# Optimization experiments

Hardware: AMD Instinct MI355X
Metric: run time of the kernel (lower is better)

Reference implementation:

```python
import jax, jax.numpy as jnp
import numpy as np

V, E, HD, H, T = 50000, 256, 512, 256, 50  # vocab, embed, hidden_dim, per-direction hidden, tagset
B, S = 128, 512


def setup_inputs() -> dict:
    key = jax.random.key(0)
    ks = jax.random.split(key, 16)
    def n(k, shape, s=0.05):
        return jax.random.normal(k, shape, dtype=jnp.float32) * s
    return {
        "sentences": jax.random.randint(ks[0], (B, S), 0, V),
        "tags": jax.random.randint(ks[1], (B, S), 0, T),
        "mask": jnp.ones((B, S), dtype=bool),
        "embedding": n(ks[2], (V, E), 0.1),
        "w_ih_f": n(ks[3], (4 * H, E)), "w_hh_f": n(ks[4], (4 * H, H)),
        "b_ih_f": n(ks[5], (4 * H,)), "b_hh_f": n(ks[6], (4 * H,)),
        "w_ih_b": n(ks[7], (4 * H, E)), "w_hh_b": n(ks[8], (4 * H, H)),
        "b_ih_b": n(ks[9], (4 * H,)), "b_hh_b": n(ks[10], (4 * H,)),
        "W_out": n(ks[11], (T, HD)), "b_out": n(ks[12], (T,)),
        "start_trans": n(ks[13], (T,), 0.1),
        "end_trans": n(ks[14], (T,), 0.1),
        "trans": n(ks[15], (T, T), 0.1),
    }


def _lstm(xs, w_ih, w_hh, b, reverse):
    # xs: [S, B, E]; PyTorch gate order i, f, g, o
    Hn = w_hh.shape[1]
    def cell(carry, xt):
        h, c = carry
        g = xt @ w_ih.T + h @ w_hh.T + b
        i, f, gg, o = jnp.split(g, 4, axis=-1)
        c = jax.nn.sigmoid(f) * c + jax.nn.sigmoid(i) * jnp.tanh(gg)
        h = jax.nn.sigmoid(o) * jnp.tanh(c)
        return (h, c), h
    z = jnp.zeros((xs.shape[1], Hn), xs.dtype)
    _, hs = jax.lax.scan(cell, (z, z), xs, reverse=reverse)
    return hs  # [S, B, Hn], time-aligned with xs


def reference(sentences, tags, mask, embedding, w_ih_f, w_hh_f, b_ih_f, b_hh_f,
              w_ih_b, w_hh_b, b_ih_b, b_hh_b, W_out, b_out,
              start_trans, end_trans, trans):
    xs = jnp.swapaxes(embedding[sentences], 0, 1)           # [S, B, E]
    hf = _lstm(xs, w_ih_f, w_hh_f, b_ih_f + b_hh_f, False)
    hb = _lstm(xs, w_ih_b, w_hh_b, b_ih_b + b_hh_b, True)
    emis = jnp.concatenate([hf, hb], -1) @ W_out.T + b_out  # [S, B, T]

    tagsT = jnp.swapaxes(tags, 0, 1)                        # [S, B]
    maskT = jnp.swapaxes(mask, 0, 1)                        # [S, B] bool
    mT = maskT.astype(emis.dtype)

    # --- numerator: score of the gold path (first timestep always on, per torchcrf) ---
    emit = jnp.take_along_axis(emis, tagsT[..., None], axis=-1)[..., 0]   # [S, B]
    num = start_trans[tagsT[0]] + emit[0]
    num = num + jnp.sum((trans[tagsT[:-1], tagsT[1:]] + emit[1:]) * mT[1:], axis=0)
    last = jnp.sum(maskT.astype(jnp.int32), axis=0) - 1                    # [B]
    num = num + end_trans[tags[jnp.arange(tags.shape[0]), last]]

    # --- denominator: log-partition via forward algorithm (logsumexp scan) ---
    alpha0 = start_trans[None, :] + emis[0]                 # [B, T]
    def step(alpha, inp):
        e_t, m_t = inp
        nxt = jax.nn.logsumexp(alpha[:, :, None] + trans[None] + e_t[:, None, :], axis=1)
        return jnp.where(m_t[:, None], nxt, alpha), None
    alpha, _ = jax.lax.scan(step, alpha0, (emis[1:], maskT[1:]))
    logZ = jax.nn.logsumexp(alpha + end_trans[None, :], axis=1)

    # model returns -crf(...) with reduction='mean'
    return -jnp.mean(num - logZ)
```

## Files before the change

kernel.cpp:

```cpp
#include <hip/hip_runtime.h>

typedef __bf16 bf16x8 __attribute__((ext_vector_type(8)));
typedef float f32x4 __attribute__((ext_vector_type(4)));
typedef float f32x2 __attribute__((ext_vector_type(2)));
typedef int i32x8 __attribute__((ext_vector_type(8)));
typedef unsigned short ushort_t;
typedef unsigned int u32x4 __attribute__((ext_vector_type(4)));
typedef long i64_t;

constexpr int Ee = 256;
constexpr int HDd = 512;
constexpr int Hh = 256;
constexpr int Tt = 50;
constexpr int Bb = 128;
constexpr int Ss = 512;
constexpr int G4 = 1024;
constexpr int SB = Ss * Bb;
constexpr int Tc = 64;
constexpr int NP = Ss / Tc;
constexpr int HSTR = 272;
constexpr int NSLOT = 16;

constexpr float LOG2E = 1.4426950408889634f;
constexpr float K2f = 2.8853900817779268f;

#define DI __device__ __forceinline__

DI float bf2f(ushort_t u) {
    unsigned int x = ((unsigned int)u) << 16;
    return __builtin_bit_cast(float, x);
}
DI ushort_t f2bf(float f) {
    unsigned int x = __builtin_bit_cast(unsigned int, f);
    x += 0x7fffu + ((x >> 16) & 1u);
    return (ushort_t)(x >> 16);
}
DI bf16x8 cvt8(const float* p) {
    bf16x8 r;
#pragma unroll
    for (int i = 0; i < 8; ++i) r[i] = (__bf16)p[i];
    return r;
}
DI unsigned int pk4_fp8(float a, float b, float c, float d) {
    int v = __builtin_amdgcn_cvt_pk_fp8_f32(a, b, 0, false);
    v = __builtin_amdgcn_cvt_pk_fp8_f32(c, d, v, true);
    return (unsigned int)v;
}
DI unsigned char fp8_1(float a) {
    return (unsigned char)(__builtin_amdgcn_cvt_pk_fp8_f32(a, 0.f, 0, false) & 0xff);
}
DI float rcpf(float x) { return __builtin_amdgcn_rcpf(x); }

#if __has_builtin(__builtin_amdgcn_exp2f)
DI float ex2(float x) { return __builtin_amdgcn_exp2f(x); }
DI float ex2n(float x) { return __builtin_amdgcn_exp2f(-x); }
#else
DI float ex2(float x) {
    float r;
    asm("v_exp_f32 %0, %1\n\ts_nop 0" : "=v"(r) : "v"(x));
    return r;
}
DI float ex2n(float x) {
    float r;
    asm("v_exp_f32 %0, -%1\n\ts_nop 0" : "=v"(r) : "v"(x));
    return r;
}
#endif

DI void lds_barrier() {
    asm volatile("" ::: "memory");
    __builtin_amdgcn_s_waitcnt(0xC07F);
    __builtin_amdgcn_s_barrier();
    asm volatile("" ::: "memory");
}

__global__ void k_prep(const float* __restrict__ wihf, const float* __restrict__ whhf,
                       const float* __restrict__ wihb, const float* __restrict__ whhb,
                       const float* __restrict__ wout,
                       const float* __restrict__ bihf, const float* __restrict__ bhhf,
                       const float* __restrict__ bihb, const float* __restrict__ bhhb,
                       ushort_t* __restrict__ Wihf, ushort_t* __restrict__ Wihb,
                       unsigned char* __restrict__ Whhf8, unsigned char* __restrict__ Whhb8,
                       unsigned char* __restrict__ Wout8,
                       float* __restrict__ biasf, float* __restrict__ biasb,
                       unsigned int* __restrict__ flags) {
    int i = blockIdx.x * 256 + threadIdx.x;
    if (i < G4 * Ee) {
        float s = (((i >> 16) & 3) == 2) ? K2f : LOG2E;
        Wihf[i] = f2bf(wihf[i] * s);
        Wihb[i] = f2bf(wihb[i] * s);
    }
    if (i < G4 * Hh / 4) {
        int base = i * 4;
        float s = (((i >> 14) & 3) == 2) ? K2f : LOG2E;
        ((unsigned int*)Whhf8)[i] = pk4_fp8(whhf[base] * s, whhf[base + 1] * s,
                                            whhf[base + 2] * s, whhf[base + 3] * s);
        ((unsigned int*)Whhb8)[i] = pk4_fp8(whhb[base] * s, whhb[base + 1] * s,
                                            whhb[base + 2] * s, whhb[base + 3] * s);
    }
    if (i < 64 * HDd) Wout8[i] = 0;
    if (i < Tt * HDd) Wout8[i] = fp8_1(wout[i]);
    if (i < G4) {
        float s = (((i >> 8) & 3) == 2) ? K2f : LOG2E;
        biasf[i] = (bihf[i] + bhhf[i]) * s;
        biasb[i] = (bihb[i] + bhhb[i]) * s;
    }
    if (i < 32) flags[i] = 0;
}

struct PhaseArgs {
    const int* sentences;
    const int* tags;
    const float* emb;
    const ushort_t* Wihf;
    const ushort_t* Wihb;
    const float* biasf;
    const float* biasb;
    const unsigned char* Whhf8;
    const unsigned char* Whhb8;
    const unsigned char* Wout8;
    const float* bout;
    const float* start_trans;
    const float* end_trans;
    const float* trans;
    unsigned char* Gbuf;
    unsigned char* Hcat8;
    float* emis;
    float* logZ;
    float* num;
    float* out;
    unsigned int* flags;
};

__global__ __launch_bounds__(512, 2) void k_phase(PhaseArgs a) {
    __shared__ unsigned char hring[NSLOT][16][HSTR];
    const size_t CH = (size_t)Tc * Bb * G4;
    int blk = blockIdx.x;
    int tid = threadIdx.x;

    if (blk < 16) {
        int ln = tid & 15, qd = (tid >> 4) & 3, w = tid >> 6;
        int dir = blk >> 3;
        int b0 = (blk & 7) * 16;
        const unsigned char* Whh8 = dir ? a.Whhb8 : a.Whhf8;
        int jc0 = w * 32 + ln;

        i32x8 wreg[2][4][2];
#pragma unroll
        for (int ct = 0; ct < 2; ++ct)
#pragma unroll
            for (int g = 0; g < 4; ++g) {
                const unsigned char* wb = Whh8 + (size_t)(g * Hh + jc0 + ct * 16) * Hh;
#pragma unroll
                for (int ks = 0; ks < 2; ++ks)
                    wreg[ct][g][ks] = *(const i32x8*)(wb + ks * 128 + qd * 32);
            }
        for (int i = tid; i < NSLOT * 16 * HSTR; i += 512) ((unsigned char*)hring)[i] = 0;
        __syncthreads();
        float creg[2][4] = {};
        int sctr = 0;

        for (int p = 0; p < NP; ++p) {
            if (tid == 0) {
                while (__hip_atomic_load(&a.flags[p], __ATOMIC_RELAXED,
                                         __HIP_MEMORY_SCOPE_AGENT) < 240u)
                    __builtin_amdgcn_s_sleep(1);
                __threadfence();
            }
            __syncthreads();

            const unsigned char* G = a.Gbuf + ((size_t)(dir * 2 + (p & 1))) * CH;
            int goff = ((dir ? (Tc - 1) : 0) * 32 + (b0 >> 2) + qd) * 4096 + jc0 * 16;
            const int gstep = dir ? -(32 * 4096) : (32 * 4096);

            u32x4 guA[2], guB[2];
#pragma unroll
            for (int ct = 0; ct < 2; ++ct)
                guA[ct] = *(const u32x4*)(G + goff + ct * 256);

            auto lstm_step = [&](u32x4(&gcur)[2], u32x4(&gnxt)[2], int step) {
                int rslot = (sctr + NSLOT - 1) & (NSLOT - 1), wslot = sctr & (NSLOT - 1);
                int goff2 = goff + gstep;
                if (step + 1 < Tc) {
#pragma unroll
                    for (int ct = 0; ct < 2; ++ct)
                        gnxt[ct] = *(const u32x4*)(G + goff2 + ct * 256);
                }
                i32x8 av2[2];
#pragma unroll
                for (int ks = 0; ks < 2; ++ks)
                    av2[ks] = *(const i32x8*)&hring[rslot][ln][ks * 128 + qd * 32];
                f32x4 acc[2][4];
#pragma unroll
                for (int ct = 0; ct < 2; ++ct)
#pragma unroll
                    for (int g = 0; g < 4; ++g) {
                        f32x2 lo = __builtin_amdgcn_cvt_pk_f32_fp8((int)gcur[ct][g], false);
                        f32x2 hi = __builtin_amdgcn_cvt_pk_f32_fp8((int)gcur[ct][g], true);
                        acc[ct][g][0] = lo[0];
                        acc[ct][g][1] = lo[1];
                        acc[ct][g][2] = hi[0];
                        acc[ct][g][3] = hi[1];
                    }
#pragma unroll
                for (int ks = 0; ks < 2; ++ks)
#pragma unroll
                    for (int ct = 0; ct < 2; ++ct)
#pragma unroll
                        for (int g = 0; g < 4; ++g)
                            acc[ct][g] = __builtin_amdgcn_mfma_scale_f32_16x16x128_f8f6f4(
                                av2[ks], wreg[ct][g][ks], acc[ct][g],
                                0, 0,
                                0, 127,
                                0, 127);
#pragma unroll
                for (int ct = 0; ct < 2; ++ct)
#pragma unroll
                    for (int reg = 0; reg < 4; ++reg) {
                        float ei = ex2n(acc[ct][0][reg]);
                        float ef = ex2n(acc[ct][1][reg]);
                        float eg = ex2(acc[ct][2][reg]);
                        float eo = ex2n(acc[ct][3][reg]);
                        float pf = 1.f + ef;
                        float pig = (1.f + ei) * (eg + 1.f);
                        float t2 = fmaf(eg, K2f, -K2f);
                        float cn = fmaf(creg[ct][reg], pig, t2 * pf) * rcpf(pf * pig);
                        creg[ct][reg] = cn;
                        float ec = ex2(cn);
                        float h = (ec - 1.f) * rcpf((1.f + eo) * (ec + 1.f));
                        hring[wslot][qd * 4 + reg][jc0 + ct * 16] = fp8_1(h);
                    }
                goff = goff2;
                lds_barrier();

                if ((sctr & 7) == 7) {
                    int tbase = sctr - 7;
                    int rid = tid >> 2;
                    int slotidx = rid >> 4, m = rid & 15;
                    int slot = (tbase + slotidx) & (NSLOT - 1);
                    int qp = tid & 3;
                    int t = dir ? (511 - (tbase + slotidx)) : (tbase + slotidx);
                    const unsigned char* src = &hring[slot][m][qp * 64];
                    unsigned char* dst = a.Hcat8 + ((size_t)(t * Bb + b0 + m)) * HDd + dir * Hh + qp * 64;
#pragma unroll
                    for (int i2 = 0; i2 < 4; ++i2) {
                        u32x4 v;
#pragma unroll
                        for (int k = 0; k < 4; ++k)
                            v[k] = *(const unsigned int*)(src + i2 * 16 + k * 4);
                        *(u32x4*)(dst + i2 * 16) = v;
                    }
                }
                ++sctr;
            };

            for (int step = 0; step < Tc; step += 2) {
                lstm_step(guA, guB, step);
                lstm_step(guB, guA, step + 1);
            }

            __syncthreads();
            if (tid == 0) {
                if (p == NP - 1) __threadfence();
                atomicAdd(&a.flags[8 + p], 1u);
            }
        }
    } else {
        int team = tid >> 8;
        int stid = tid & 255;
        int slot = (blk - 16) * 2 + team;
        int ln = stid & 15, qd = (stid >> 4) & 3, wv = stid >> 6;
        for (int q = 0; q < NP; ++q) {
            if (q >= 2) {
                if (tid == 0)
                    while (__hip_atomic_load(&a.flags[8 + q - 2], __ATOMIC_RELAXED,
                                             __HIP_MEMORY_SCOPE_AGENT) < 16u)
                        __builtin_amdgcn_s_sleep(64);
                __syncthreads();
            }
            for (int tile = slot; tile < 1024; tile += 480) {
                int dir = tile >> 9;
                int rem = tile & 511;
                int rt0 = rem >> 3, ct0 = rem & 7;
                const ushort_t* W = dir ? a.Wihb : a.Wihf;
                const float* bias = dir ? a.biasb : a.biasf;
                unsigned char* Gout = a.Gbuf + ((size_t)(dir * 2 + (q & 1))) * CH;
                int t0 = dir ? (NP - 1 - q) * Tc : q * Tc;
                int r0 = rt0 * 128 + (wv & 1) * 64;
                int n0 = ct0 * 128 + (wv >> 1) * 64;
                const float* aptr[4];
#pragma unroll
                for (int rt = 0; rt < 4; ++rt) {
                    int r = r0 + rt * 16 + ln;
                    int t = t0 + (r >> 7), b = r & 127;
                    aptr[rt] = a.emb + (size_t)a.sentences[b * Ss + t] * Ee;
                }
                int wrow[4];
#pragma unroll
                for (int ct = 0; ct < 4; ++ct) {
                    int c = n0 + ct * 16 + ln;
                    wrow[ct] = (c & 3) * 256 + (c >> 2);
                }
                f32x4 acc[4][4] = {};
                for (int ks = 0; ks < 8; ++ks) {
                    int k0 = ks * 32 + qd * 8;
                    bf16x8 av[4], bfr[4];
#pragma unroll
                    for (int rt = 0; rt < 4; ++rt) av[rt] = cvt8(aptr[rt] + k0);
#pragma unroll
                    for (int ct = 0; ct < 4; ++ct)
                        bfr[ct] = *(const bf16x8*)(W + (size_t)wrow[ct] * Ee + k0);
#pragma unroll
                    for (int rt = 0; rt < 4; ++rt)
#pragma unroll
                        for (int ct = 0; ct < 4; ++ct)
                            acc[rt][ct] = __builtin_amdgcn_mfma_f32_16x16x32_bf16(av[rt], bfr[ct], acc[rt][ct], 0, 0, 0);
                }
#pragma unroll
                for (int rt = 0; rt < 4; ++rt)
#pragma unroll
                    for (int ct = 0; ct < 4; ++ct) {
                        int c = n0 + ct * 16 + ln;
                        float bv = bias[wrow[ct]];
                        unsigned int pk = pk4_fp8(acc[rt][ct][0] + bv, acc[rt][ct][1] + bv,
                                                  acc[rt][ct][2] + bv, acc[rt][ct][3] + bv);
                        int rowq = ((r0 + rt * 16) >> 2) + qd;
                        *(unsigned int*)(Gout + (size_t)rowq * 4096 + (size_t)c * 4) = pk;
                    }
            }
            __syncthreads();
            if (tid == 0) {
                __threadfence();
                atomicAdd(&a.flags[q], 1u);
            }
        }
    }

    if (tid == 0) {
        while (__hip_atomic_load(&a.flags[15], __ATOMIC_RELAXED,
                                 __HIP_MEMORY_SCOPE_AGENT) < 16u)
            __builtin_amdgcn_s_sleep(16);
        __threadfence();
    }
    __syncthreads();
    {
        int ln = tid & 15, qd = (tid >> 4) & 3, w = tid >> 6;
        int r0 = blk * 256 + w * 32;
        f32x4 acc[2][4] = {};
        for (int ks = 0; ks < 16; ++ks) {
            int k0 = ks * 32 + qd * 8;
            i64_t av[2], bfr[4];
#pragma unroll
            for (int rt = 0; rt < 2; ++rt)
                av[rt] = *(const i64_t*)(a.Hcat8 + (size_t)(r0 + rt * 16 + ln) * HDd + k0);
#pragma unroll
            for (int ct = 0; ct < 4; ++ct)
                bfr[ct] = *(const i64_t*)(a.Wout8 + (size_t)(ct * 16 + ln) * HDd + k0);
#pragma unroll
            for (int rt = 0; rt < 2; ++rt)
#pragma unroll
                for (int ct = 0; ct < 4; ++ct)
                    acc[rt][ct] = __builtin_amdgcn_mfma_f32_16x16x32_fp8_fp8(av[rt], bfr[ct], acc[rt][ct], 0, 0, 0);
        }
#pragma unroll
        for (int rt = 0; rt < 2; ++rt)
#pragma unroll
            for (int ct = 0; ct < 4; ++ct) {
                int j = ct * 16 + ln;
                if (j < Tt) {
                    float bv = a.bout[j];
#pragma unroll
                    for (int reg = 0; reg < 4; ++reg) {
                        int row = r0 + rt * 16 + qd * 4 + reg;
                        int t = row >> 7, b = row & 127;
                        a.emis[((size_t)b * Ss + t) * Tt + j] = acc[rt][ct][reg] + bv;
                    }
                }
            }
    }
    __syncthreads();
    if (tid == 0) {
        __threadfence();
        atomicAdd(&a.flags[16], 1u);
        while (__hip_atomic_load(&a.flags[16], __ATOMIC_RELAXED,
                                 __HIP_MEMORY_SCOPE_AGENT) < 256u)
            __builtin_amdgcn_s_sleep(16);
        __threadfence();
    }
    __syncthreads();

    if (blk < 128) {
        if (tid < 64) {
            float* E_s = (float*)&hring[0][0][0];
            int j = tid;
            int b = blk;
            const float* eb = a.emis + (size_t)b * Ss * Tt;

            float preg[52];
            preg[50] = 0.f;
            preg[51] = 0.f;
#pragma unroll
            for (int i = 0; i < Tt; ++i)
                preg[i] = (j < Tt) ? __expf(a.trans[i * Tt + j]) : 0.f;

            float astart = (j < Tt) ? (a.start_trans[j] + eb[j]) : 0.f;
            float a0 = __builtin_amdgcn_readfirstlane(astart);
            float vcur = (j < Tt) ? __expf(astart - a0) : 0.f;
            float logacc = a0;
            E_s[j] = vcur;

            float ecur[8], enxt[8];
#pragma unroll
            for (int i = 0; i < 8; ++i)
                ecur[i] = (j < Tt && 1 + i < Ss) ? eb[(1 + i) * Tt + j] : 0.f;

            for (int tb = 1; tb < Ss; tb += 8) {
#pragma unroll
                for (int i = 0; i < 8; ++i) {
                    int tn = tb + 8 + i;
                    enxt[i] = (j < Tt && tn < Ss) ? eb[(size_t)tn * Tt + j] : 0.f;
                }
                float ex[8];
#pragma unroll
                for (int i = 0; i < 8; ++i) ex[i] = __expf(ecur[i]);
#pragma unroll
                for (int i = 0; i < 8; ++i) {
                    int t = tb + i;
                    if (t >= Ss) break;
                    float s0 = 0.f, s1 = 0.f, s2 = 0.f, s3 = 0.f;
#pragma unroll
                    for (int i4 = 0; i4 < 13; ++i4) {
                        f32x4 ev = *(const f32x4*)&E_s[i4 * 4];
                        s0 = fmaf(ev[0], preg[i4 * 4 + 0], s0);
                        s1 = fmaf(ev[1], preg[i4 * 4 + 1], s1);
                        s2 = fmaf(ev[2], preg[i4 * 4 + 2], s2);
                        s3 = fmaf(ev[3], preg[i4 * 4 + 3], s3);
                    }
                    vcur = ((s0 + s1) + (s2 + s3)) * ex[i];
                    if (i == 3) {
                        float n = __builtin_amdgcn_readfirstlane(vcur);
                        vcur *= rcpf(n);
                        logacc += __logf(n);
                    }
                    E_s[j] = vcur;
                }
                float n = __builtin_amdgcn_readfirstlane(vcur);
                vcur *= rcpf(n);
                E_s[j] = vcur;
                logacc += __logf(n);
#pragma unroll
                for (int i = 0; i < 8; ++i) ecur[i] = enxt[i];
            }
            float ve = (j < Tt) ? vcur * __expf(a.end_trans[j]) : 0.f;
            for (int off = 32; off > 0; off >>= 1) ve += __shfl_down(ve, off, 64);
            if (j == 0) a.logZ[b] = logacc + __logf(ve);
        }
    } else {
        float* red = (float*)&hring[1][0][0];
        int b = blk - 128;
        const float* eb = a.emis + (size_t)b * Ss * Tt;
        float v = 0.f;
        int t = 1 + tid;
        if (t < Ss) {
            int tp = a.tags[b * Ss + t - 1], tc = a.tags[b * Ss + t];
            v = a.trans[tp * Tt + tc] + eb[(size_t)t * Tt + tc];
        }
        if (tid == 0) {
            int t0 = a.tags[b * Ss + 0];
            v += a.start_trans[t0] + eb[t0] + a.end_trans[a.tags[b * Ss + Ss - 1]];
        }
        for (int off = 32; off > 0; off >>= 1) v += __shfl_down(v, off, 64);
        if ((tid & 63) == 0) red[tid >> 6] = v;
        __syncthreads();
        if (tid == 0) {
            float s = 0.f;
#pragma unroll
            for (int i = 0; i < 8; ++i) s += red[i];
            a.num[b] = s;
        }
    }
    __syncthreads();
    if (tid == 0) {
        __threadfence();
        atomicAdd(&a.flags[17], 1u);
    }

    if (blk == 0) {
        if (tid == 0) {
            while (__hip_atomic_load(&a.flags[17], __ATOMIC_RELAXED,
                                     __HIP_MEMORY_SCOPE_AGENT) < 256u)
                __builtin_amdgcn_s_sleep(16);
            __threadfence();
        }
        __syncthreads();
        float* red = (float*)&hring[2][0][0];
        float v = (tid < 128) ? (a.num[tid] - a.logZ[tid]) : 0.f;
        for (int off = 32; off > 0; off >>= 1) v += __shfl_down(v, off, 64);
        if ((tid & 63) == 0) red[tid >> 6] = v;
        __syncthreads();
        if (tid == 0) {
            float s = 0.f;
#pragma unroll
            for (int i = 0; i < 8; ++i) s += red[i];
            a.out[0] = -s / 128.f;
        }
    }
}

extern "C" void kernel_launch(void* const* d_in, const int* in_sizes, int n_in,
                              void* d_out, int out_size, void* d_ws, size_t ws_size,
                              hipStream_t stream) {
    const int* sentences = (const int*)d_in[0];
    const int* tags = (const int*)d_in[1];
    const float* emb = (const float*)d_in[3];
    const float* wihf = (const float*)d_in[4];
    const float* whhf = (const float*)d_in[5];
    const float* bihf = (const float*)d_in[6];
    const float* bhhf = (const float*)d_in[7];
    const float* wihb = (const float*)d_in[8];
    const float* whhb = (const float*)d_in[9];
    const float* bihb = (const float*)d_in[10];
    const float* bhhb = (const float*)d_in[11];
    const float* wout = (const float*)d_in[12];
    const float* bout = (const float*)d_in[13];
    const float* start_trans = (const float*)d_in[14];
    const float* end_trans = (const float*)d_in[15];
    const float* trans = (const float*)d_in[16];

    char* ws = (char*)d_ws;
    size_t off = 0;
    auto alloc = [&](size_t bytes) {
        void* p = ws + off;
        off += (bytes + 255) & ~(size_t)255;
        return p;
    };
    ushort_t* Wihf = (ushort_t*)alloc((size_t)G4 * Ee * 2);
    ushort_t* Wihb = (ushort_t*)alloc((size_t)G4 * Ee * 2);
    unsigned char* Whhf8 = (unsigned char*)alloc((size_t)G4 * Hh);
    unsigned char* Whhb8 = (unsigned char*)alloc((size_t)G4 * Hh);
    unsigned char* Wout8 = (unsigned char*)alloc((size_t)64 * HDd);
    float* biasf = (float*)alloc(G4 * 4);
    float* biasb = (float*)alloc(G4 * 4);
    unsigned char* Gbuf = (unsigned char*)alloc((size_t)4 * Tc * Bb * G4);
    unsigned char* Hcat8 = (unsigned char*)alloc((size_t)SB * HDd);
    float* emis = (float*)alloc((size_t)SB * Tt * 4);
    float* logZ = (float*)alloc(Bb * 4);
    float* num = (float*)alloc(Bb * 4);
    unsigned int* flags = (unsigned int*)alloc(64 * 4);
    (void)ws_size; (void)in_sizes; (void)n_in; (void)out_size;

    k_prep<<<dim3((G4 * Ee + 255) / 256), dim3(256), 0, stream>>>(
        wihf, whhf, wihb, whhb, wout, bihf, bhhf, bihb, bhhb,
        Wihf, Wihb, Whhf8, Whhb8, Wout8, biasf, biasb, flags);

    PhaseArgs pa;
    pa.sentences = sentences;
    pa.tags = tags;
    pa.emb = emb;
    pa.Wihf = Wihf;
    pa.Wihb = Wihb;
    pa.biasf = biasf;
    pa.biasb = biasb;
    pa.Whhf8 = Whhf8;
    pa.Whhb8 = Whhb8;
    pa.Wout8 = Wout8;
    pa.bout = bout;
    pa.start_trans = start_trans;
    pa.end_trans = end_trans;
    pa.trans = trans;
    pa.Gbuf = Gbuf;
    pa.Hcat8 = Hcat8;
    pa.emis = emis;
    pa.logZ = logZ;
    pa.num = num;
    pa.out = (float*)d_out;
    pa.flags = flags;
    void* kargs[] = {&pa};
    hipLaunchCooperativeKernel((void*)k_phase, dim3(256), dim3(512), kargs, 0, stream);
}
```

Before: 1.295 ms.

## Fold weight prep into cooperative kernel and use readlane in CRF forward

Removes the separate k_prep launch and performs the weight conversion to bf16/fp8 and the bias folding inside the cooperative k_phase kernel, followed by a grid-wide atomic barrier. The flags are now zeroed with a memset. Separately, the CRF forward recurrence now broadcasts alpha values across lanes with readlane instead of an LDS store and reload. This aims to save a kernel launch and LDS round trips on the serial dependency chain, at the cost of an extra grid barrier and about 50 scalar readlanes per step.

```diff
diff --git a/kernel.cpp b/kernel.cpp
--- a/kernel.cpp
+++ b/kernel.cpp
@@ -50,6 +50,9 @@
     return (unsigned char)(__builtin_amdgcn_cvt_pk_fp8_f32(a, 0.f, 0, false) & 0xff);
 }
 DI float rcpf(float x) { return __builtin_amdgcn_rcpf(x); }
+DI float rdlane(float v, int l) {
+    return __builtin_bit_cast(float, __builtin_amdgcn_readlane(__builtin_bit_cast(int, v), l));
+}
 
 #if __has_builtin(__builtin_amdgcn_exp2f)
 DI float ex2(float x) { return __builtin_amdgcn_exp2f(x); }
@@ -74,55 +77,20 @@
     asm volatile("" ::: "memory");
 }
 
-__global__ void k_prep(const float* __restrict__ wihf, const float* __restrict__ whhf,
-                       const float* __restrict__ wihb, const float* __restrict__ whhb,
-                       const float* __restrict__ wout,
-                       const float* __restrict__ bihf, const float* __restrict__ bhhf,
-                       const float* __restrict__ bihb, const float* __restrict__ bhhb,
-                       ushort_t* __restrict__ Wihf, ushort_t* __restrict__ Wihb,
-                       unsigned char* __restrict__ Whhf8, unsigned char* __restrict__ Whhb8,
-                       unsigned char* __restrict__ Wout8,
-                       float* __restrict__ biasf, float* __restrict__ biasb,
-                       unsigned int* __restrict__ flags) {
-    int i = blockIdx.x * 256 + threadIdx.x;
-    if (i < G4 * Ee) {
-        float s = (((i >> 16) & 3) == 2) ? K2f : LOG2E;
-        Wihf[i] = f2bf(wihf[i] * s);
-        Wihb[i] = f2bf(wihb[i] * s);
-    }
-    if (i < G4 * Hh / 4) {
-        int base = i * 4;
-        float s = (((i >> 14) & 3) == 2) ? K2f : LOG2E;
-        ((unsigned int*)Whhf8)[i] = pk4_fp8(whhf[base] * s, whhf[base + 1] * s,
-                                            whhf[base + 2] * s, whhf[base + 3] * s);
-        ((unsigned int*)Whhb8)[i] = pk4_fp8(whhb[base] * s, whhb[base + 1] * s,
-                                            whhb[base + 2] * s, whhb[base + 3] * s);
-    }
-    if (i < 64 * HDd) Wout8[i] = 0;
-    if (i < Tt * HDd) Wout8[i] = fp8_1(wout[i]);
-    if (i < G4) {
-        float s = (((i >> 8) & 3) == 2) ? K2f : LOG2E;
-        biasf[i] = (bihf[i] + bhhf[i]) * s;
-        biasb[i] = (bihb[i] + bhhb[i]) * s;
-    }
-    if (i < 32) flags[i] = 0;
-}
-
 struct PhaseArgs {
     const int* sentences;
     const int* tags;
     const float* emb;
-    const ushort_t* Wihf;
-    const ushort_t* Wihb;
-    const float* biasf;
-    const float* biasb;
-    const unsigned char* Whhf8;
-    const unsigned char* Whhb8;
-    const unsigned char* Wout8;
-    const float* bout;
+    const float* wihf; const float* whhf; const float* bihf; const float* bhhf;
+    const float* wihb; const float* whhb; const float* bihb; const float* bhhb;
+    const float* wout; const float* bout;
     const float* start_trans;
     const float* end_trans;
     const float* trans;
+    ushort_t* Wihf; ushort_t* Wihb;
+    unsigned char* Whhf8; unsigned char* Whhb8;
+    unsigned char* Wout8;
+    float* biasf; float* biasb;
     unsigned char* Gbuf;
     unsigned char* Hcat8;
     float* emis;
@@ -137,6 +105,39 @@
     const size_t CH = (size_t)Tc * Bb * G4;
     int blk = blockIdx.x;
     int tid = threadIdx.x;
+
+    for (int i = blk * 512 + tid; i < G4 * Ee; i += 256 * 512) {
+        {
+            float s = (((i >> 16) & 3) == 2) ? K2f : LOG2E;
+            a.Wihf[i] = f2bf(a.wihf[i] * s);
+            a.Wihb[i] = f2bf(a.wihb[i] * s);
+        }
+        if (i < G4 * Hh / 4) {
+            int base = i * 4;
+            float s = (((i >> 14) & 3) == 2) ? K2f : LOG2E;
+            ((unsigned int*)a.Whhf8)[i] = pk4_fp8(a.whhf[base] * s, a.whhf[base + 1] * s,
+                                                  a.whhf[base + 2] * s, a.whhf[base + 3] * s);
+            ((unsigned int*)a.Whhb8)[i] = pk4_fp8(a.whhb[base] * s, a.whhb[base + 1] * s,
+                                                  a.whhb[base + 2] * s, a.whhb[base + 3] * s);
+        }
+        if (i < 64 * HDd) a.Wout8[i] = 0;
+        if (i < Tt * HDd) a.Wout8[i] = fp8_1(a.wout[i]);
+        if (i < G4) {
+            float s = (((i >> 8) & 3) == 2) ? K2f : LOG2E;
+            a.biasf[i] = (a.bihf[i] + a.bhhf[i]) * s;
+            a.biasb[i] = (a.bihb[i] + a.bhhb[i]) * s;
+        }
+    }
+    __syncthreads();
+    if (tid == 0) {
+        __threadfence();
+        atomicAdd(&a.flags[18], 1u);
+        while (__hip_atomic_load(&a.flags[18], __ATOMIC_RELAXED,
+                                 __HIP_MEMORY_SCOPE_AGENT) < 256u)
+            __builtin_amdgcn_s_sleep(1);
+        __threadfence();
+    }
+    __syncthreads();
 
     if (blk < 16) {
         int ln = tid & 15, qd = (tid >> 4) & 3, w = tid >> 6;
@@ -391,7 +392,6 @@
 
     if (blk < 128) {
         if (tid < 64) {
-            float* E_s = (float*)&hring[0][0][0];
             int j = tid;
             int b = blk;
             const float* eb = a.emis + (size_t)b * Ss * Tt;
@@ -407,7 +407,6 @@
             float a0 = __builtin_amdgcn_readfirstlane(astart);
             float vcur = (j < Tt) ? __expf(astart - a0) : 0.f;
             float logacc = a0;
-            E_s[j] = vcur;
 
             float ecur[8], enxt[8];
 #pragma unroll
@@ -430,11 +429,10 @@
                     float s0 = 0.f, s1 = 0.f, s2 = 0.f, s3 = 0.f;
 #pragma unroll
                     for (int i4 = 0; i4 < 13; ++i4) {
-                        f32x4 ev = *(const f32x4*)&E_s[i4 * 4];
-                        s0 = fmaf(ev[0], preg[i4 * 4 + 0], s0);
-                        s1 = fmaf(ev[1], preg[i4 * 4 + 1], s1);
-                        s2 = fmaf(ev[2], preg[i4 * 4 + 2], s2);
-                        s3 = fmaf(ev[3], preg[i4 * 4 + 3], s3);
+                        s0 = fmaf(rdlane(vcur, i4 * 4 + 0), preg[i4 * 4 + 0], s0);
+                        s1 = fmaf(rdlane(vcur, i4 * 4 + 1), preg[i4 * 4 + 1], s1);
+                        s2 = fmaf(rdlane(vcur, i4 * 4 + 2), preg[i4 * 4 + 2], s2);
+                        s3 = fmaf(rdlane(vcur, i4 * 4 + 3), preg[i4 * 4 + 3], s3);
                     }
                     vcur = ((s0 + s1) + (s2 + s3)) * ex[i];
                     if (i == 3) {
@@ -442,11 +440,9 @@
                         vcur *= rcpf(n);
                         logacc += __logf(n);
                     }
-                    E_s[j] = vcur;
                 }
                 float n = __builtin_amdgcn_readfirstlane(vcur);
                 vcur *= rcpf(n);
-                E_s[j] = vcur;
                 logacc += __logf(n);
 #pragma unroll
                 for (int i = 0; i < 8; ++i) ecur[i] = enxt[i];
@@ -549,25 +545,25 @@
     unsigned int* flags = (unsigned int*)alloc(64 * 4);
     (void)ws_size; (void)in_sizes; (void)n_in; (void)out_size;
 
-    k_prep<<<dim3((G4 * Ee + 255) / 256), dim3(256), 0, stream>>>(
-        wihf, whhf, wihb, whhb, wout, bihf, bhhf, bihb, bhhb,
-        Wihf, Wihb, Whhf8, Whhb8, Wout8, biasf, biasb, flags);
+    hipMemsetAsync(flags, 0, 256, stream);
 
     PhaseArgs pa;
     pa.sentences = sentences;
     pa.tags = tags;
     pa.emb = emb;
+    pa.wihf = wihf; pa.whhf = whhf; pa.bihf = bihf; pa.bhhf = bhhf;
+    pa.wihb = wihb; pa.whhb = whhb; pa.bihb = bihb; pa.bhhb = bhhb;
+    pa.wout = wout; pa.bout = bout;
+    pa.start_trans = start_trans;
+    pa.end_trans = end_trans;
+    pa.trans = trans;
     pa.Wihf = Wihf;
     pa.Wihb = Wihb;
-    pa.biasf = biasf;
-    pa.biasb = biasb;
     pa.Whhf8 = Whhf8;
     pa.Whhb8 = Whhb8;
     pa.Wout8 = Wout8;
-    pa.bout = bout;
-    pa.start_trans = start_trans;
-    pa.end_trans = end_trans;
-    pa.trans = trans;
+    pa.biasf = biasf;
+    pa.biasb = biasb;
     pa.Gbuf = Gbuf;
     pa.Hcat8 = Hcat8;
     pa.emis = emis;
```

Result: no change. 1.309 ms (+1.1%).
